# Kernel optimization log

Hardware: AMD Instinct MI355X
Metric: run time of the kernel (lower is better)

## Reference

```python
import jax, jax.numpy as jnp
import numpy as np

H = 16          # num_heads (init kwarg)
EPS = 1e-6      # LayerNorm eps


def rope_freqs(L, d):
    # interleaved RoPE freqs, repeat(f, 'i j -> i (j r)', r=2)
    t = jnp.arange(L, dtype=jnp.float32)
    inv = 1.0 / (10000.0 ** (jnp.arange(0, d, 2, dtype=jnp.float32) / d))
    f = t[:, None] * inv[None, :]          # (L, d//2)
    return jnp.repeat(f, 2, axis=-1)       # (L, d)


def rotate_half(x):
    # pair adjacent elems: (x1, x2) -> (-x2, x1)
    shp = x.shape
    x = x.reshape(shp[:-1] + (shp[-1] // 2, 2))
    x1, x2 = x[..., 0], x[..., 1]
    return jnp.stack((-x2, x1), axis=-1).reshape(shp)


def apply_rope(x, f):
    # x: (B, H, L, d), f: (L, d)
    return x * jnp.cos(f) + rotate_half(x) * jnp.sin(f)


def layernorm(x, g, b):
    m = jnp.mean(x, axis=-1, keepdims=True)
    v = jnp.mean(jnp.square(x - m), axis=-1, keepdims=True)
    return (x - m) * jax.lax.rsqrt(v + EPS) * g + b


def setup_inputs() -> dict:
    key = jax.random.key(0)
    ks = jax.random.split(key, 12)
    B, L, D = 2, 2048, 1024
    Dff = 4 * D
    s = 0.02
    inp = {
        'x': jax.random.normal(ks[0], (B, L, D), jnp.float32),
        'ln1_g': jnp.ones((D,), jnp.float32),
        'ln1_b': jnp.zeros((D,), jnp.float32),
        'wq': jax.random.normal(ks[1], (D, D), jnp.float32) * s,
        'bq': jnp.zeros((D,), jnp.float32),
        'wk': jax.random.normal(ks[2], (D, D), jnp.float32) * s,
        'bk': jnp.zeros((D,), jnp.float32),
        'wv': jax.random.normal(ks[3], (D, D), jnp.float32) * s,
        'bv': jnp.zeros((D,), jnp.float32),
        'wo': jax.random.normal(ks[4], (D, D), jnp.float32) * s,
        'bo': jnp.zeros((D,), jnp.float32),
        'ln2_g': jnp.ones((D,), jnp.float32),
        'ln2_b': jnp.zeros((D,), jnp.float32),
        'w1': jax.random.normal(ks[5], (D, Dff), jnp.float32) * s,
        'b1': jnp.zeros((Dff,), jnp.float32),
        'w2': jax.random.normal(ks[6], (Dff, D), jnp.float32) * s,
        'b2': jnp.zeros((D,), jnp.float32),
        # gates are zero-init in the module; use small random so the block is exercised
        'gate_msa': jax.random.normal(ks[7], (1, 1, D), jnp.float32) * 0.1,
        'gate_mlp': jax.random.normal(ks[8], (1, 1, D), jnp.float32) * 0.1,
    }
    return inp


def reference(x, ln1_g, ln1_b, wq, bq, wk, bk, wv, bv, wo, bo,
              ln2_g, ln2_b, w1, b1, w2, b2, gate_msa, gate_mlp):
    B, L, D = x.shape
    hd = D // H
    # --- self-attention branch ---
    h = layernorm(x, ln1_g, ln1_b)
    q = (h @ wq + bq).reshape(B, L, H, hd).transpose(0, 2, 1, 3)  # (B,H,L,hd)
    k = (h @ wk + bk).reshape(B, L, H, hd).transpose(0, 2, 1, 3)
    v = (h @ wv + bv).reshape(B, L, H, hd).transpose(0, 2, 1, 3)
    f = rope_freqs(L, hd)
    q = apply_rope(q, f)
    k = apply_rope(k, f)
    scores = jnp.einsum('bhic,bhjc->bhij', q, k) / np.float32(np.sqrt(hd))
    attn = jax.nn.softmax(scores, axis=-1)  # dropout disabled (eval)
    o = jnp.einsum('bhij,bhjc->bhic', attn, v)
    o = o.transpose(0, 2, 1, 3).reshape(B, L, D)
    x = x + gate_msa * (o @ wo + bo)
    # --- gated MLP branch ---
    h2 = layernorm(x, ln2_g, ln2_b)
    mlp = jax.nn.gelu(h2 @ w1 + b1, approximate=False) @ w2 + b2
    return x + gate_mlp * mlp
```

## Files before the change

kernel.cpp:

```cpp
#include <hip/hip_runtime.h>

typedef unsigned short u16;
typedef __attribute__((ext_vector_type(4))) float f32x4;
typedef __attribute__((ext_vector_type(16))) float f32x16;
typedef __attribute__((ext_vector_type(8))) short bf16x8;

#define DEV static __device__ __forceinline__

DEV float bf2f(u16 u) { unsigned int i = ((unsigned int)u) << 16; return __builtin_bit_cast(float, i); }
DEV u16 f2bf(float f) {
  unsigned int x = __builtin_bit_cast(unsigned int, f);
  x += 0x7fffu + ((x >> 16) & 1u);
  return (u16)(x >> 16);
}

DEV unsigned cvtpk(float lo, float hi) {
  unsigned r;
  asm("v_cvt_pk_bf16_f32 %0, %1, %2" : "=v"(r) : "v"(lo), "v"(hi));
  return r;
}
DEV float exp2a(float x) {
  float r;
  asm("v_exp_f32 %0, %1" : "=v"(r) : "v"(x));
  return r;
}

template <int N>
DEV void wait_vmcnt() {
  if constexpr (N == 0) asm volatile("s_waitcnt vmcnt(0)" ::: "memory");
  else if constexpr (N == 3) asm volatile("s_waitcnt vmcnt(3)" ::: "memory");
  else if constexpr (N == 4) asm volatile("s_waitcnt vmcnt(4)" ::: "memory");
  else static_assert(N == 0, "unsupported vmcnt");
}

DEV void gload16(const u16* g, u16* l) {
  __builtin_amdgcn_global_load_lds(
      (const __attribute__((address_space(1))) unsigned int*)g,
      (__attribute__((address_space(3))) unsigned int*)l, 16, 0, 0);
}

__global__ __launch_bounds__(256) void ln_k(const float* __restrict__ x,
                                            const float* __restrict__ g,
                                            const float* __restrict__ b,
                                            u16* __restrict__ out) {
  const int row = blockIdx.x;
  const int t = threadIdx.x;
  const float4 v = *(const float4*)(x + (size_t)row * 1024 + t * 4);
  float s = v.x + v.y + v.z + v.w;
  float q = v.x * v.x + v.y * v.y + v.z * v.z + v.w * v.w;
#pragma unroll
  for (int m = 1; m < 64; m <<= 1) { s += __shfl_xor(s, m); q += __shfl_xor(q, m); }
  __shared__ float ss[4], qs[4];
  if ((t & 63) == 0) { ss[t >> 6] = s; qs[t >> 6] = q; }
  __syncthreads();
  s = ss[0] + ss[1] + ss[2] + ss[3];
  q = qs[0] + qs[1] + qs[2] + qs[3];
  const float mean = s * (1.0f / 1024.0f);
  const float var = q * (1.0f / 1024.0f) - mean * mean;
  const float rs = rsqrtf(var + 1e-6f);
  const float4 gv = *(const float4*)(g + t * 4);
  const float4 bv = *(const float4*)(b + t * 4);
  ushort4 o;
  o.x = f2bf((v.x - mean) * rs * gv.x + bv.x);
  o.y = f2bf((v.y - mean) * rs * gv.y + bv.y);
  o.z = f2bf((v.z - mean) * rs * gv.z + bv.z);
  o.w = f2bf((v.w - mean) * rs * gv.w + bv.w);
  *(ushort4*)(out + (size_t)row * 1024 + t * 4) = o;
}

__global__ __launch_bounds__(256) void tcvt_k(const float* __restrict__ src,
                                              u16* __restrict__ dst, int K, int N) {
  __shared__ u16 tl[32][33];
  const int k0 = blockIdx.x * 32, n0 = blockIdx.y * 32;
  const int c = threadIdx.x & 31, r0 = threadIdx.x >> 5;
#pragma unroll
  for (int p = 0; p < 4; p++) {
    const int r = p * 8 + r0;
    tl[r][c] = f2bf(src[(size_t)(k0 + r) * N + n0 + c]);
  }
  __syncthreads();
#pragma unroll
  for (int p = 0; p < 4; p++) {
    const int r = p * 8 + r0;
    dst[(size_t)(n0 + r) * K + k0 + c] = tl[c][r];
  }
}

template <int EPI, int TN>
__global__ __launch_bounds__(256) void gemm_bt(const u16* __restrict__ A,
                                               const u16* __restrict__ Bt,
                                               const float* __restrict__ bias,
                                               const float* __restrict__ resid,
                                               const float* __restrict__ gate,
                                               void* __restrict__ outv,
                                               int M, int N, int K) {
  constexpr int MI = (TN == 128) ? 4 : 2;
  constexpr int WRS = (TN == 128) ? 64 : 32;
  constexpr int L = 2 + TN / 64;
  __shared__ __align__(16) u16 lA[3][128 * 32];
  __shared__ __align__(16) u16 lB[3][TN * 32];
  const int tid = threadIdx.x;
  const int lane = tid & 63, wid = tid >> 6;
  const int l4 = lane >> 4, l15 = lane & 15;
  const int wr = (TN == 128) ? (wid >> 1) : wid;
  const int wc = (TN == 128) ? (wid & 1) : 0;
  const int mBase = blockIdx.x * 128;
  const int nBase = blockIdx.y * TN;

  f32x4 acc[MI][4];
#pragma unroll
  for (int i = 0; i < MI; i++)
#pragma unroll
    for (int j = 0; j < 4; j++)
#pragma unroll
      for (int e = 0; e < 4; e++) acc[i][j][e] = 0.f;

  const int sRow = tid >> 2;
  const int sCol = (((tid & 3) ^ ((sRow >> 1) & 3))) * 8;
  const int rsw = (l15 >> 1) & 3;

#define STAGE(bufi, k0)                                                               \
  {                                                                                   \
    _Pragma("unroll") for (int p = 0; p < 2; p++)                                     \
        gload16(A + (size_t)(mBase + p * 64 + sRow) * K + (k0) + sCol,                \
                &lA[bufi][p * 2048 + wid * 512]);                                     \
    _Pragma("unroll") for (int p = 0; p < TN / 64; p++)                               \
        gload16(Bt + (size_t)(nBase + p * 64 + sRow) * K + (k0) + sCol,               \
                &lB[bufi][p * 2048 + wid * 512]);                                     \
  }

  const int nt = K >> 5;
  STAGE(0, 0);
  STAGE(1, 32);
  wait_vmcnt<L>();
  __builtin_amdgcn_s_barrier();
  __builtin_amdgcn_sched_barrier(0);

  int bsel = 0;
  for (int it = 0; it < nt; ++it) {
    bf16x8 af[MI], bfr[4];
#pragma unroll
    for (int mi = 0; mi < MI; mi++)
      af[mi] = *(const bf16x8*)(&lA[bsel][(wr * WRS + mi * 16 + l15) * 32 + (l4 ^ rsw) * 8]);
#pragma unroll
    for (int ni = 0; ni < 4; ni++)
      bfr[ni] = *(const bf16x8*)(&lB[bsel][(wc * 64 + ni * 16 + l15) * 32 + (l4 ^ rsw) * 8]);
    if (it + 2 < nt) {
      int b2 = bsel + 2; if (b2 >= 3) b2 -= 3;
      STAGE(b2, (it + 2) * 32);
    }
#pragma unroll
    for (int mi = 0; mi < MI; mi++)
#pragma unroll
      for (int ni = 0; ni < 4; ni++)
        acc[mi][ni] = __builtin_amdgcn_mfma_f32_16x16x32_bf16(af[mi], bfr[ni], acc[mi][ni], 0, 0, 0);
    if (it + 1 < nt) {
      asm volatile("s_waitcnt lgkmcnt(0)" ::: "memory");
      __builtin_amdgcn_sched_barrier(0);
      if (it + 2 < nt) wait_vmcnt<L>();
      else wait_vmcnt<0>();
      __builtin_amdgcn_s_barrier();
      __builtin_amdgcn_sched_barrier(0);
    }
    bsel = (bsel == 2) ? 0 : bsel + 1;
  }
#undef STAGE

  u16* obf = (u16*)outv;
  float* of = (float*)outv;
#pragma unroll
  for (int mi = 0; mi < MI; mi++) {
#pragma unroll
    for (int ni = 0; ni < 4; ni++) {
      const int row0 = mBase + wr * WRS + mi * 16 + l4 * 4;
      const int col = nBase + wc * 64 + ni * 16 + l15;
      const float bb = bias[col];
#pragma unroll
      for (int r = 0; r < 4; r++) {
        const float v = acc[mi][ni][r] + bb;
        const size_t idx = (size_t)(row0 + r) * N + col;
        if (EPI == 0) {
          obf[idx] = f2bf(v);
        } else if (EPI == 1) {
          const float ge = 0.5f * v * (1.0f + erff(v * 0.70710678118654752f));
          obf[idx] = f2bf(ge);
        } else if (EPI == 2) {
          of[idx] = resid[idx] + gate[col] * v;
        } else {
          of[idx] = of[idx] + gate[col] * v;
        }
      }
    }
  }
}

__global__ __launch_bounds__(256) void rope_k(const u16* __restrict__ qkv,
                                              u16* __restrict__ qr, u16* __restrict__ kr) {
  const int sel = blockIdx.y;
  const int rid = blockIdx.x * 8 + (threadIdx.x >> 5);
  const int i = threadIdx.x & 31;
  const int b = rid >> 15;
  const int h = (rid >> 11) & 15;
  const int t = rid & 2047;
  const u16* src = qkv + (size_t)(b * 2048 + t) * 3072 + sel * 1024 + h * 64 + 2 * i;
  const ushort2 uv = *(const ushort2*)src;
  const float x0 = bf2f(uv.x), x1 = bf2f(uv.y);
  const float inv = __expf(-(float)i * 0.28782313662425572f);
  float sn, cs;
  sincosf((float)t * inv, &sn, &cs);
  const float sc = sel ? 1.0f : 0.18033688011112042f;
  ushort2 ov;
  ov.x = f2bf((x0 * cs - x1 * sn) * sc);
  ov.y = f2bf((x1 * cs + x0 * sn) * sc);
  *(ushort2*)((sel ? kr : qr) + (size_t)rid * 64 + 2 * i) = ov;
}

__global__ __launch_bounds__(256) void vtrans_k(const u16* __restrict__ qkv, u16* __restrict__ vt) {
  __shared__ u16 tl[64][65];
  const int bh = blockIdx.x >> 5;
  const int t0 = (blockIdx.x & 31) * 64;
  const int b = bh >> 4, h = bh & 15;
  const int tid = threadIdx.x;
#pragma unroll
  for (int p = 0; p < 16; p++) {
    const int e = p * 256 + tid;
    const int tr = e >> 6, d = e & 63;
    tl[tr][d] = qkv[(size_t)(b * 2048 + t0 + tr) * 3072 + 2048 + h * 64 + d];
  }
  __syncthreads();
#pragma unroll
  for (int p = 0; p < 16; p++) {
    const int e = p * 256 + tid;
    const int dr = e >> 6, tc = e & 63;
    vt[(size_t)(bh * 64 + dr) * 2048 + t0 + tc] = tl[tc][dr];
  }
}

__global__ __launch_bounds__(256) void attn_k(const u16* __restrict__ q,
                                              const u16* __restrict__ k,
                                              const u16* __restrict__ vt,
                                              u16* __restrict__ o) {
  const int bh = blockIdx.y;
  const int tid = threadIdx.x;
  const int wid = tid >> 6, lane = tid & 63;
  const int h = lane >> 5, rq = lane & 31;
  const int qrow0 = blockIdx.x * 128 + wid * 32;

  __shared__ __align__(16) u16 kls[2][4096];
  __shared__ __align__(16) u16 vls[2][4096];
  __shared__ __align__(16) float alds[4][32];

  const u16* qbase = q + ((size_t)bh * 2048 + qrow0 + rq) * 64 + 8 * h;
  bf16x8 qf[4];
#pragma unroll
  for (int db = 0; db < 4; db++) qf[db] = *(const bf16x8*)(qbase + db * 16);

  float m0 = -1e30f, ls0 = 0.f;
  f32x16 oacc0, oacc1;
#pragma unroll
  for (int e = 0; e < 16; e++) { oacc0[e] = 0.f; oacc1[e] = 0.f; }

  const char* kg = (const char*)(k + (size_t)bh * 2048 * 64);
  const char* vg = (const char*)(vt + (size_t)bh * 64 * 2048);
  const int sA = tid, sB = 256 + tid;
  const int rA = sA >> 3, cA = ((sA & 7) ^ (rA & 7)) << 4;
  const int rB = sB >> 3, cB = ((sB & 7) ^ (rB & 7)) << 4;
  u16* kd0 = &kls[0][(size_t)(wid * 64) * 8];
  u16* kd1 = &kls[0][(size_t)(256 + wid * 64) * 8];
  u16* vd0 = &vls[0][(size_t)(wid * 64) * 8];
  u16* vd1 = &vls[0][(size_t)(256 + wid * 64) * 8];

#define STAGE(bufi, kv0)                                                            \
  {                                                                                 \
    const int _o = (bufi)*4096;                                                     \
    gload16((const u16*)(kg + (size_t)((kv0) + rA) * 128 + cA), kd0 + _o);          \
    gload16((const u16*)(kg + (size_t)((kv0) + rB) * 128 + cB), kd1 + _o);          \
    gload16((const u16*)(vg + (size_t)rA * 4096 + (kv0)*2 + cA), vd0 + _o);         \
    gload16((const u16*)(vg + (size_t)rB * 4096 + (kv0)*2 + cB), vd1 + _o);         \
  }

  STAGE(0, 0);
  __syncthreads();

  float* AL = alds[wid];
  const int swz = (rq & 7) << 4;

#define PACK8(S, B, OUT)                                                            \
  {                                                                                 \
    unsigned wA = cvtpk(S[B + 0], S[B + 1]), wB_ = cvtpk(S[B + 2], S[B + 3]);       \
    unsigned wC = cvtpk(S[B + 4], S[B + 5]), wD = cvtpk(S[B + 6], S[B + 7]);        \
    unsigned xA = __shfl_xor(wA, 32), xB = __shfl_xor(wB_, 32);                     \
    unsigned xC = __shfl_xor(wC, 32), xD = __shfl_xor(wD, 32);                      \
    union { unsigned u[4]; bf16x8 v; } _m;                                          \
    _m.u[0] = h ? xC : wA; _m.u[1] = h ? xD : wB_;                                  \
    _m.u[2] = h ? wC : xA; _m.u[3] = h ? wD : xB;                                   \
    OUT = _m.v;                                                                     \
  }

  int buf = 0;
  for (int it = 0; it < 32; ++it) {
    if (it < 31) STAGE(buf ^ 1, (it + 1) * 64);
    const char* K = (const char*)kls[buf];
    const char* V = (const char*)vls[buf];

    f32x16 st0, st1;
#pragma unroll
    for (int e = 0; e < 16; e++) { st0[e] = 0.f; st1[e] = 0.f; }
#pragma unroll
    for (int db = 0; db < 4; db++) {
      const int cb = db * 32;
      const bf16x8 ka0 = *(const bf16x8*)(K + rq * 128 + ((cb + 16 * h) ^ swz));
      const bf16x8 ka1 = *(const bf16x8*)(K + (32 + rq) * 128 + ((cb + 16 * h) ^ swz));
      st0 = __builtin_amdgcn_mfma_f32_32x32x16_bf16(ka0, qf[db], st0, 0, 0, 0);
      st1 = __builtin_amdgcn_mfma_f32_32x32x16_bf16(ka1, qf[db], st1, 0, 0, 0);
    }

    float t0 = fmaxf(fmaxf(st0[0], st0[1]), fmaxf(st0[2], st0[3]));
    float t1 = fmaxf(fmaxf(st0[4], st0[5]), fmaxf(st0[6], st0[7]));
    float t2 = fmaxf(fmaxf(st0[8], st0[9]), fmaxf(st0[10], st0[11]));
    float t3 = fmaxf(fmaxf(st0[12], st0[13]), fmaxf(st0[14], st0[15]));
    float t4 = fmaxf(fmaxf(st1[0], st1[1]), fmaxf(st1[2], st1[3]));
    float t5 = fmaxf(fmaxf(st1[4], st1[5]), fmaxf(st1[6], st1[7]));
    float t6 = fmaxf(fmaxf(st1[8], st1[9]), fmaxf(st1[10], st1[11]));
    float t7 = fmaxf(fmaxf(st1[12], st1[13]), fmaxf(st1[14], st1[15]));
    float pm = fmaxf(fmaxf(fmaxf(t0, t1), fmaxf(t2, t3)), fmaxf(fmaxf(t4, t5), fmaxf(t6, t7)));
    pm = fmaxf(pm, __shfl_xor(pm, 32));
    const bool need = !__all(pm <= m0 + 11.54f);
    float al0 = 1.0f;
    if (need) {
      const float mn = fmaxf(m0, pm);
      al0 = exp2a(m0 - mn);
      m0 = mn;
    }
#pragma unroll
    for (int e = 0; e < 16; e++) {
      st0[e] = exp2a(st0[e] - m0);
      st1[e] = exp2a(st1[e] - m0);
    }
    float u0 = (st0[0] + st0[1]) + (st0[2] + st0[3]);
    float u1 = (st0[4] + st0[5]) + (st0[6] + st0[7]);
    float u2 = (st0[8] + st0[9]) + (st0[10] + st0[11]);
    float u3 = (st0[12] + st0[13]) + (st0[14] + st0[15]);
    float u4 = (st1[0] + st1[1]) + (st1[2] + st1[3]);
    float u5 = (st1[4] + st1[5]) + (st1[6] + st1[7]);
    float u6 = (st1[8] + st1[9]) + (st1[10] + st1[11]);
    float u7 = (st1[12] + st1[13]) + (st1[14] + st1[15]);
    float ps = ((u0 + u1) + (u2 + u3)) + ((u4 + u5) + (u6 + u7));
    ps += __shfl_xor(ps, 32);
    ls0 = ls0 * al0 + ps;

    if (need) {
      if (lane < 32) AL[rq] = al0;
      const f32x4 a0 = *(const f32x4*)((const char*)AL + 16 * h);
      const f32x4 a1 = *(const f32x4*)((const char*)AL + 32 + 16 * h);
      const f32x4 a2 = *(const f32x4*)((const char*)AL + 64 + 16 * h);
      const f32x4 a3 = *(const f32x4*)((const char*)AL + 96 + 16 * h);
#pragma unroll
      for (int r = 0; r < 4; r++) {
        oacc0[r] *= a0[r]; oacc0[4 + r] *= a1[r]; oacc0[8 + r] *= a2[r]; oacc0[12 + r] *= a3[r];
        oacc1[r] *= a0[r]; oacc1[4 + r] *= a1[r]; oacc1[8 + r] *= a2[r]; oacc1[12 + r] *= a3[r];
      }
    }

    bf16x8 pa[4];
    PACK8(st0, 0, pa[0]);
    PACK8(st0, 8, pa[1]);
    PACK8(st1, 0, pa[2]);
    PACK8(st1, 8, pa[3]);

#pragma unroll
    for (int kb = 0; kb < 4; kb++) {
      const int cb = kb * 32;
      const bf16x8 vb0 = *(const bf16x8*)(V + rq * 128 + ((cb + 16 * h) ^ swz));
      const bf16x8 vb1 = *(const bf16x8*)(V + (32 + rq) * 128 + ((cb + 16 * h) ^ swz));
      oacc0 = __builtin_amdgcn_mfma_f32_32x32x16_bf16(pa[kb], vb0, oacc0, 0, 0, 0);
      oacc1 = __builtin_amdgcn_mfma_f32_32x32x16_bf16(pa[kb], vb1, oacc1, 0, 0, 0);
    }
    __syncthreads();
    buf ^= 1;
  }
#undef STAGE
#undef PACK8

  if (lane < 32) AL[rq] = 1.0f / ls0;
  f32x4 ivg[4];
  ivg[0] = *(const f32x4*)((const char*)AL + 16 * h);
  ivg[1] = *(const f32x4*)((const char*)AL + 32 + 16 * h);
  ivg[2] = *(const f32x4*)((const char*)AL + 64 + 16 * h);
  ivg[3] = *(const f32x4*)((const char*)AL + 96 + 16 * h);
  const int b = bh >> 4, hh = bh & 15;
#pragma unroll
  for (int r = 0; r < 16; r++) {
    const int qa = qrow0 + (r & 3) + 8 * (r >> 2) + 4 * h;
    u16* orow = o + ((size_t)b * 2048 + qa) * 1024 + hh * 64;
    const float iv = ivg[r >> 2][r & 3];
    orow[rq] = f2bf(oacc0[r] * iv);
    orow[32 + rq] = f2bf(oacc1[r] * iv);
  }
}

extern "C" void kernel_launch(void* const* d_in, const int* in_sizes, int n_in,
                              void* d_out, int out_size, void* d_ws, size_t ws_size,
                              hipStream_t stream) {
  (void)in_sizes; (void)n_in; (void)out_size; (void)ws_size;
  const float* x     = (const float*)d_in[0];
  const float* ln1_g = (const float*)d_in[1];
  const float* ln1_b = (const float*)d_in[2];
  const float* wq    = (const float*)d_in[3];
  const float* bq    = (const float*)d_in[4];
  const float* wk    = (const float*)d_in[5];
  const float* bk    = (const float*)d_in[6];
  const float* wv    = (const float*)d_in[7];
  const float* bv    = (const float*)d_in[8];
  const float* wo    = (const float*)d_in[9];
  const float* bo    = (const float*)d_in[10];
  const float* ln2_g = (const float*)d_in[11];
  const float* ln2_b = (const float*)d_in[12];
  const float* w1    = (const float*)d_in[13];
  const float* b1    = (const float*)d_in[14];
  const float* w2    = (const float*)d_in[15];
  const float* b2    = (const float*)d_in[16];
  const float* gmsa  = (const float*)d_in[17];
  const float* gmlp  = (const float*)d_in[18];
  float* out = (float*)d_out;

  char* w = (char*)d_ws;
  auto alloc = [&](size_t bytes) {
    char* p = w;
    w += (bytes + 255) & ~(size_t)255;
    return p;
  };
  u16* h1     = (u16*)alloc(4096UL * 1024 * 2);
  u16* wqkv_t = (u16*)alloc(3072UL * 1024 * 2);
  u16* wo_t   = (u16*)alloc(1024UL * 1024 * 2);
  u16* w1_t   = (u16*)alloc(4096UL * 1024 * 2);
  u16* w2_t   = (u16*)alloc(1024UL * 4096 * 2);
  float* bqkv = (float*)alloc(3072UL * 4);
  u16* qkv    = (u16*)alloc(4096UL * 3072 * 2);
  u16* q_r    = (u16*)alloc(65536UL * 64 * 2);
  u16* k_r    = (u16*)alloc(65536UL * 64 * 2);
  u16* v_t    = (u16*)alloc(65536UL * 64 * 2);
  u16* o_at   = (u16*)alloc(4096UL * 1024 * 2);
  u16* h2     = (u16*)alloc(4096UL * 1024 * 2);
  u16* g1     = (u16*)alloc(4096UL * 4096 * 2);

  tcvt_k<<<dim3(32, 32), 256, 0, stream>>>(wq, wqkv_t, 1024, 1024);
  tcvt_k<<<dim3(32, 32), 256, 0, stream>>>(wk, wqkv_t + 1024 * 1024, 1024, 1024);
  tcvt_k<<<dim3(32, 32), 256, 0, stream>>>(wv, wqkv_t + 2048 * 1024, 1024, 1024);
  tcvt_k<<<dim3(32, 32), 256, 0, stream>>>(wo, wo_t, 1024, 1024);
  tcvt_k<<<dim3(32, 128), 256, 0, stream>>>(w1, w1_t, 1024, 4096);
  tcvt_k<<<dim3(128, 32), 256, 0, stream>>>(w2, w2_t, 4096, 1024);
  hipMemcpyAsync(bqkv,        bq, 1024 * sizeof(float), hipMemcpyDeviceToDevice, stream);
  hipMemcpyAsync(bqkv + 1024, bk, 1024 * sizeof(float), hipMemcpyDeviceToDevice, stream);
  hipMemcpyAsync(bqkv + 2048, bv, 1024 * sizeof(float), hipMemcpyDeviceToDevice, stream);

  ln_k<<<4096, 256, 0, stream>>>(x, ln1_g, ln1_b, h1);
  gemm_bt<0, 128><<<dim3(32, 24), 256, 0, stream>>>(h1, wqkv_t, bqkv, nullptr, nullptr, qkv, 4096, 3072, 1024);
  rope_k<<<dim3(8192, 2), 256, 0, stream>>>(qkv, q_r, k_r);
  vtrans_k<<<1024, 256, 0, stream>>>(qkv, v_t);
  attn_k<<<dim3(16, 32), 256, 0, stream>>>(q_r, k_r, v_t, o_at);
  gemm_bt<2, 64><<<dim3(32, 16), 256, 0, stream>>>(o_at, wo_t, bo, x, gmsa, out, 4096, 1024, 1024);

  ln_k<<<4096, 256, 0, stream>>>(out, ln2_g, ln2_b, h2);
  gemm_bt<1, 128><<<dim3(32, 32), 256, 0, stream>>>(h2, w1_t, b1, nullptr, nullptr, g1, 4096, 4096, 1024);
  gemm_bt<3, 64><<<dim3(32, 16), 256, 0, stream>>>(g1, w2_t, b2, nullptr, gmlp, out, 4096, 1024, 4096);
}
```

Measured before the change: 286.3 us.

## Split attention KV range across two warp groups and merge softmax partials

The attention block grows to 512 threads: two groups of four waves each process half of the key/value sequence for the same 128 query rows, with separate double-buffered LDS tiles. At the end, group 1 writes its partial output, max and sum to shared memory, and group 0 rescales and combines both partials before storing. The aim is more waves per CU and a shorter serial KV loop for the 512-block grid. In exchange it doubles LDS use per block and adds a combine step with an extra barrier.

```diff
diff --git a/kernel.cpp b/kernel.cpp
--- a/kernel.cpp
+++ b/kernel.cpp
@@ -236,19 +236,22 @@
   }
 }
 
-__global__ __launch_bounds__(256) void attn_k(const u16* __restrict__ q,
+__global__ __launch_bounds__(512) void attn_k(const u16* __restrict__ q,
                                               const u16* __restrict__ k,
                                               const u16* __restrict__ vt,
                                               u16* __restrict__ o) {
   const int bh = blockIdx.y;
   const int tid = threadIdx.x;
-  const int wid = tid >> 6, lane = tid & 63;
+  const int grp = tid >> 8;
+  const int wid = (tid >> 6) & 3;
+  const int lane = tid & 63;
   const int h = lane >> 5, rq = lane & 31;
   const int qrow0 = blockIdx.x * 128 + wid * 32;
 
-  __shared__ __align__(16) u16 kls[2][4096];
-  __shared__ __align__(16) u16 vls[2][4096];
-  __shared__ __align__(16) float alds[4][32];
+  __shared__ __align__(16) u16 kls[2][2][4096];
+  __shared__ __align__(16) u16 vls[2][2][4096];
+  __shared__ __align__(16) float alds[8][32];
+  __shared__ __align__(16) float mls[4][32], lls[4][32];
 
   const u16* qbase = q + ((size_t)bh * 2048 + qrow0 + rq) * 64 + 8 * h;
   bf16x8 qf[4];
@@ -262,13 +265,17 @@
 
   const char* kg = (const char*)(k + (size_t)bh * 2048 * 64);
   const char* vg = (const char*)(vt + (size_t)bh * 64 * 2048);
-  const int sA = tid, sB = 256 + tid;
+  const int t8 = tid & 255;
+  const int sA = t8, sB = 256 + t8;
   const int rA = sA >> 3, cA = ((sA & 7) ^ (rA & 7)) << 4;
   const int rB = sB >> 3, cB = ((sB & 7) ^ (rB & 7)) << 4;
-  u16* kd0 = &kls[0][(size_t)(wid * 64) * 8];
-  u16* kd1 = &kls[0][(size_t)(256 + wid * 64) * 8];
-  u16* vd0 = &vls[0][(size_t)(wid * 64) * 8];
-  u16* vd1 = &vls[0][(size_t)(256 + wid * 64) * 8];
+  u16* kgrp = &kls[grp][0][0];
+  u16* vgrp = &vls[grp][0][0];
+  u16* kd0 = kgrp + wid * 512;
+  u16* kd1 = kgrp + 2048 + wid * 512;
+  u16* vd0 = vgrp + wid * 512;
+  u16* vd1 = vgrp + 2048 + wid * 512;
+  const int kvbase = grp * 1024;
 
 #define STAGE(bufi, kv0)                                                            \
   {                                                                                 \
@@ -279,10 +286,10 @@
     gload16((const u16*)(vg + (size_t)rB * 4096 + (kv0)*2 + cB), vd1 + _o);         \
   }
 
-  STAGE(0, 0);
+  STAGE(0, kvbase);
   __syncthreads();
 
-  float* AL = alds[wid];
+  float* AL = alds[tid >> 6];
   const int swz = (rq & 7) << 4;
 
 #define PACK8(S, B, OUT)                                                            \
@@ -298,10 +305,10 @@
   }
 
   int buf = 0;
-  for (int it = 0; it < 32; ++it) {
-    if (it < 31) STAGE(buf ^ 1, (it + 1) * 64);
-    const char* K = (const char*)kls[buf];
-    const char* V = (const char*)vls[buf];
+  for (int it = 0; it < 16; ++it) {
+    if (it < 15) STAGE(buf ^ 1, kvbase + (it + 1) * 64);
+    const char* K = (const char*)(kgrp + buf * 4096);
+    const char* V = (const char*)(vgrp + buf * 4096);
 
     f32x16 st0, st1;
 #pragma unroll
@@ -382,20 +389,41 @@
 #undef STAGE
 #undef PACK8
 
-  if (lane < 32) AL[rq] = 1.0f / ls0;
-  f32x4 ivg[4];
-  ivg[0] = *(const f32x4*)((const char*)AL + 16 * h);
-  ivg[1] = *(const f32x4*)((const char*)AL + 32 + 16 * h);
-  ivg[2] = *(const f32x4*)((const char*)AL + 64 + 16 * h);
-  ivg[3] = *(const f32x4*)((const char*)AL + 96 + 16 * h);
-  const int b = bh >> 4, hh = bh & 15;
-#pragma unroll
-  for (int r = 0; r < 16; r++) {
-    const int qa = qrow0 + (r & 3) + 8 * (r >> 2) + 4 * h;
-    u16* orow = o + ((size_t)b * 2048 + qa) * 1024 + hh * 64;
-    const float iv = ivg[r >> 2][r & 3];
-    orow[rq] = f2bf(oacc0[r] * iv);
-    orow[32 + rq] = f2bf(oacc1[r] * iv);
+  float* comb = (float*)&kls[0][0][0];
+  if (grp == 1) {
+    if (lane < 32) { mls[wid][rq] = m0; lls[wid][rq] = ls0; }
+    float* cw = comb + wid * 2048;
+#pragma unroll
+    for (int r = 0; r < 16; r++) {
+      const int ql = (r & 3) + 8 * (r >> 2) + 4 * h;
+      cw[ql * 64 + rq] = oacc0[r];
+      cw[ql * 64 + 32 + rq] = oacc1[r];
+    }
+  }
+  __syncthreads();
+  if (grp == 0) {
+    const float mb = mls[wid][rq], lb = lls[wid][rq];
+    const float M = fmaxf(m0, mb);
+    const float sa = exp2a(m0 - M), sb = exp2a(mb - M);
+    const float linv = 1.0f / (ls0 * sa + lb * sb);
+    if (lane < 32) { AL[rq] = sa * linv; mls[wid][rq] = sb * linv; }
+    asm volatile("s_waitcnt lgkmcnt(0)" ::: "memory");
+    f32x4 fa[4], fb[4];
+#pragma unroll
+    for (int g = 0; g < 4; g++) {
+      fa[g] = *(const f32x4*)((const char*)AL + g * 32 + 16 * h);
+      fb[g] = *(const f32x4*)((const char*)&mls[wid][0] + g * 32 + 16 * h);
+    }
+    const float* cw = comb + wid * 2048;
+    const int b = bh >> 4, hh = bh & 15;
+#pragma unroll
+    for (int r = 0; r < 16; r++) {
+      const int ql = (r & 3) + 8 * (r >> 2) + 4 * h;
+      const float A = fa[r >> 2][r & 3], B = fb[r >> 2][r & 3];
+      u16* orow = o + ((size_t)b * 2048 + qrow0 + ql) * 1024 + hh * 64;
+      orow[rq] = f2bf(oacc0[r] * A + cw[ql * 64 + rq] * B);
+      orow[32 + rq] = f2bf(oacc1[r] * A + cw[ql * 64 + 32 + rq] * B);
+    }
   }
 }
 
@@ -458,7 +486,7 @@
   gemm_bt<0, 128><<<dim3(32, 24), 256, 0, stream>>>(h1, wqkv_t, bqkv, nullptr, nullptr, qkv, 4096, 3072, 1024);
   rope_k<<<dim3(8192, 2), 256, 0, stream>>>(qkv, q_r, k_r);
   vtrans_k<<<1024, 256, 0, stream>>>(qkv, v_t);
-  attn_k<<<dim3(16, 32), 256, 0, stream>>>(q_r, k_r, v_t, o_at);
+  attn_k<<<dim3(16, 32), 512, 0, stream>>>(q_r, k_r, v_t, o_at);
   gemm_bt<2, 64><<<dim3(32, 16), 256, 0, stream>>>(o_at, wo_t, bo, x, gmsa, out, 4096, 1024, 1024);
 
   ln_k<<<4096, 256, 0, stream>>>(out, ln2_g, ln2_b, h2);
```

Measured after the change: 284.1 us. No clear change (-0.8%).

## Load K tiles straight into registers and double-buffer them across attention iterations

Applied to the files above, without the earlier changes.

The attention kernel no longer stages K through LDS. Each wave reads its K fragments directly from global memory into registers, one tile ahead, while V keeps its LDS double buffer. The loop is unrolled by two with ping-pong register buffers, explicit vmcnt/lgkmcnt waits and raw s_barrier. The MFMA sections are also wrapped in s_setprio. This is meant to cut LDS traffic and barrier cost, but every wave now fetches the same K tile separately, which raises global/L2 load traffic and register pressure.

```diff
diff --git a/kernel.cpp b/kernel.cpp
--- a/kernel.cpp
+++ b/kernel.cpp
@@ -30,6 +30,7 @@
   if constexpr (N == 0) asm volatile("s_waitcnt vmcnt(0)" ::: "memory");
   else if constexpr (N == 3) asm volatile("s_waitcnt vmcnt(3)" ::: "memory");
   else if constexpr (N == 4) asm volatile("s_waitcnt vmcnt(4)" ::: "memory");
+  else if constexpr (N == 8) asm volatile("s_waitcnt vmcnt(8)" ::: "memory");
   else static_assert(N == 0, "unsupported vmcnt");
 }
 
@@ -236,6 +237,121 @@
   }
 }
 
+#define PACK8(S, B, OUT, H)                                                         \
+  {                                                                                 \
+    unsigned wA = cvtpk(S[B + 0], S[B + 1]), wB_ = cvtpk(S[B + 2], S[B + 3]);       \
+    unsigned wC = cvtpk(S[B + 4], S[B + 5]), wD = cvtpk(S[B + 6], S[B + 7]);        \
+    unsigned xA = __shfl_xor(wA, 32), xB = __shfl_xor(wB_, 32);                     \
+    unsigned xC = __shfl_xor(wC, 32), xD = __shfl_xor(wD, 32);                      \
+    union { unsigned u[4]; bf16x8 v; } _m;                                          \
+    _m.u[0] = (H) ? xC : wA; _m.u[1] = (H) ? xD : wB_;                              \
+    _m.u[2] = (H) ? wC : xA; _m.u[3] = (H) ? wD : xB;                               \
+    OUT = _m.v;                                                                     \
+  }
+
+DEV void attn_iter(bool notlast, int kvnext,
+                   const u16* kgrow, const char* vg,
+                   int rA, int cA, int rB, int cB, u16* vdst0, u16* vdst1,
+                   const char* V, int swz, int h, int rq,
+                   const bf16x8 (&qf)[4], const bf16x8 (&kcur)[2][4], bf16x8 (&knxt)[2][4],
+                   float& m0, float& ls0, f32x16& oacc0, f32x16& oacc1, float* AL) {
+  if (notlast) {
+    gload16((const u16*)(vg + (size_t)rA * 4096 + (size_t)kvnext * 2 + cA), vdst0);
+    gload16((const u16*)(vg + (size_t)rB * 4096 + (size_t)kvnext * 2 + cB), vdst1);
+    __builtin_amdgcn_sched_barrier(0);
+    const u16* kb = kgrow + (size_t)kvnext * 64;
+#pragma unroll
+    for (int db = 0; db < 4; db++) {
+      knxt[0][db] = *(const bf16x8*)(kb + db * 16);
+      knxt[1][db] = *(const bf16x8*)(kb + 32 * 64 + db * 16);
+    }
+  }
+
+  f32x16 st0, st1;
+#pragma unroll
+  for (int e = 0; e < 16; e++) { st0[e] = 0.f; st1[e] = 0.f; }
+  __builtin_amdgcn_s_setprio(1);
+#pragma unroll
+  for (int db = 0; db < 4; db++) {
+    st0 = __builtin_amdgcn_mfma_f32_32x32x16_bf16(kcur[0][db], qf[db], st0, 0, 0, 0);
+    st1 = __builtin_amdgcn_mfma_f32_32x32x16_bf16(kcur[1][db], qf[db], st1, 0, 0, 0);
+  }
+  __builtin_amdgcn_s_setprio(0);
+
+  float t0 = fmaxf(fmaxf(st0[0], st0[1]), fmaxf(st0[2], st0[3]));
+  float t1 = fmaxf(fmaxf(st0[4], st0[5]), fmaxf(st0[6], st0[7]));
+  float t2 = fmaxf(fmaxf(st0[8], st0[9]), fmaxf(st0[10], st0[11]));
+  float t3 = fmaxf(fmaxf(st0[12], st0[13]), fmaxf(st0[14], st0[15]));
+  float t4 = fmaxf(fmaxf(st1[0], st1[1]), fmaxf(st1[2], st1[3]));
+  float t5 = fmaxf(fmaxf(st1[4], st1[5]), fmaxf(st1[6], st1[7]));
+  float t6 = fmaxf(fmaxf(st1[8], st1[9]), fmaxf(st1[10], st1[11]));
+  float t7 = fmaxf(fmaxf(st1[12], st1[13]), fmaxf(st1[14], st1[15]));
+  float pm = fmaxf(fmaxf(fmaxf(t0, t1), fmaxf(t2, t3)), fmaxf(fmaxf(t4, t5), fmaxf(t6, t7)));
+  pm = fmaxf(pm, __shfl_xor(pm, 32));
+  const bool need = !__all(pm <= m0 + 11.54f);
+  float al0 = 1.0f;
+  if (need) {
+    const float mn = fmaxf(m0, pm);
+    al0 = exp2a(m0 - mn);
+    m0 = mn;
+  }
+#pragma unroll
+  for (int e = 0; e < 16; e++) {
+    st0[e] = exp2a(st0[e] - m0);
+    st1[e] = exp2a(st1[e] - m0);
+  }
+  float u0 = (st0[0] + st0[1]) + (st0[2] + st0[3]);
+  float u1 = (st0[4] + st0[5]) + (st0[6] + st0[7]);
+  float u2 = (st0[8] + st0[9]) + (st0[10] + st0[11]);
+  float u3 = (st0[12] + st0[13]) + (st0[14] + st0[15]);
+  float u4 = (st1[0] + st1[1]) + (st1[2] + st1[3]);
+  float u5 = (st1[4] + st1[5]) + (st1[6] + st1[7]);
+  float u6 = (st1[8] + st1[9]) + (st1[10] + st1[11]);
+  float u7 = (st1[12] + st1[13]) + (st1[14] + st1[15]);
+  float ps = ((u0 + u1) + (u2 + u3)) + ((u4 + u5) + (u6 + u7));
+  ps += __shfl_xor(ps, 32);
+  ls0 = ls0 * al0 + ps;
+
+  if (need) {
+    const int lane = rq + 32 * h;
+    if (lane < 32) AL[rq] = al0;
+    const f32x4 a0 = *(const f32x4*)((const char*)AL + 16 * h);
+    const f32x4 a1 = *(const f32x4*)((const char*)AL + 32 + 16 * h);
+    const f32x4 a2 = *(const f32x4*)((const char*)AL + 64 + 16 * h);
+    const f32x4 a3 = *(const f32x4*)((const char*)AL + 96 + 16 * h);
+#pragma unroll
+    for (int r = 0; r < 4; r++) {
+      oacc0[r] *= a0[r]; oacc0[4 + r] *= a1[r]; oacc0[8 + r] *= a2[r]; oacc0[12 + r] *= a3[r];
+      oacc1[r] *= a0[r]; oacc1[4 + r] *= a1[r]; oacc1[8 + r] *= a2[r]; oacc1[12 + r] *= a3[r];
+    }
+  }
+
+  bf16x8 pa[4];
+  PACK8(st0, 0, pa[0], h);
+  PACK8(st0, 8, pa[1], h);
+  PACK8(st1, 0, pa[2], h);
+  PACK8(st1, 8, pa[3], h);
+
+  __builtin_amdgcn_s_setprio(1);
+#pragma unroll
+  for (int kb = 0; kb < 4; kb++) {
+    const int cb = kb * 32;
+    const bf16x8 vb0 = *(const bf16x8*)(V + rq * 128 + ((cb + 16 * h) ^ swz));
+    const bf16x8 vb1 = *(const bf16x8*)(V + (32 + rq) * 128 + ((cb + 16 * h) ^ swz));
+    oacc0 = __builtin_amdgcn_mfma_f32_32x32x16_bf16(pa[kb], vb0, oacc0, 0, 0, 0);
+    oacc1 = __builtin_amdgcn_mfma_f32_32x32x16_bf16(pa[kb], vb1, oacc1, 0, 0, 0);
+  }
+  __builtin_amdgcn_s_setprio(0);
+
+  if (notlast) {
+    asm volatile("s_waitcnt lgkmcnt(0)" ::: "memory");
+    __builtin_amdgcn_sched_barrier(0);
+    wait_vmcnt<8>();
+    __builtin_amdgcn_s_barrier();
+    __builtin_amdgcn_sched_barrier(0);
+  }
+}
+
 __global__ __launch_bounds__(256) void attn_k(const u16* __restrict__ q,
                                               const u16* __restrict__ k,
                                               const u16* __restrict__ vt,
@@ -246,7 +362,6 @@
   const int h = lane >> 5, rq = lane & 31;
   const int qrow0 = blockIdx.x * 128 + wid * 32;
 
-  __shared__ __align__(16) u16 kls[2][4096];
   __shared__ __align__(16) u16 vls[2][4096];
   __shared__ __align__(16) float alds[4][32];
 
@@ -260,127 +375,39 @@
 #pragma unroll
   for (int e = 0; e < 16; e++) { oacc0[e] = 0.f; oacc1[e] = 0.f; }
 
-  const char* kg = (const char*)(k + (size_t)bh * 2048 * 64);
+  const u16* kgrow = k + (size_t)bh * 2048 * 64 + (size_t)rq * 64 + 8 * h;
   const char* vg = (const char*)(vt + (size_t)bh * 64 * 2048);
   const int sA = tid, sB = 256 + tid;
   const int rA = sA >> 3, cA = ((sA & 7) ^ (rA & 7)) << 4;
   const int rB = sB >> 3, cB = ((sB & 7) ^ (rB & 7)) << 4;
-  u16* kd0 = &kls[0][(size_t)(wid * 64) * 8];
-  u16* kd1 = &kls[0][(size_t)(256 + wid * 64) * 8];
-  u16* vd0 = &vls[0][(size_t)(wid * 64) * 8];
-  u16* vd1 = &vls[0][(size_t)(256 + wid * 64) * 8];
-
-#define STAGE(bufi, kv0)                                                            \
-  {                                                                                 \
-    const int _o = (bufi)*4096;                                                     \
-    gload16((const u16*)(kg + (size_t)((kv0) + rA) * 128 + cA), kd0 + _o);          \
-    gload16((const u16*)(kg + (size_t)((kv0) + rB) * 128 + cB), kd1 + _o);          \
-    gload16((const u16*)(vg + (size_t)rA * 4096 + (kv0)*2 + cA), vd0 + _o);         \
-    gload16((const u16*)(vg + (size_t)rB * 4096 + (kv0)*2 + cB), vd1 + _o);         \
-  }
-
-  STAGE(0, 0);
-  __syncthreads();
-
+  u16* vd0 = &vls[0][wid * 512];
+  u16* vd1 = &vls[0][2048 + wid * 512];
   float* AL = alds[wid];
   const int swz = (rq & 7) << 4;
-
-#define PACK8(S, B, OUT)                                                            \
-  {                                                                                 \
-    unsigned wA = cvtpk(S[B + 0], S[B + 1]), wB_ = cvtpk(S[B + 2], S[B + 3]);       \
-    unsigned wC = cvtpk(S[B + 4], S[B + 5]), wD = cvtpk(S[B + 6], S[B + 7]);        \
-    unsigned xA = __shfl_xor(wA, 32), xB = __shfl_xor(wB_, 32);                     \
-    unsigned xC = __shfl_xor(wC, 32), xD = __shfl_xor(wD, 32);                      \
-    union { unsigned u[4]; bf16x8 v; } _m;                                          \
-    _m.u[0] = h ? xC : wA; _m.u[1] = h ? xD : wB_;                                  \
-    _m.u[2] = h ? wC : xA; _m.u[3] = h ? wD : xB;                                   \
-    OUT = _m.v;                                                                     \
-  }
-
-  int buf = 0;
-  for (int it = 0; it < 32; ++it) {
-    if (it < 31) STAGE(buf ^ 1, (it + 1) * 64);
-    const char* K = (const char*)kls[buf];
-    const char* V = (const char*)vls[buf];
-
-    f32x16 st0, st1;
-#pragma unroll
-    for (int e = 0; e < 16; e++) { st0[e] = 0.f; st1[e] = 0.f; }
-#pragma unroll
-    for (int db = 0; db < 4; db++) {
-      const int cb = db * 32;
-      const bf16x8 ka0 = *(const bf16x8*)(K + rq * 128 + ((cb + 16 * h) ^ swz));
-      const bf16x8 ka1 = *(const bf16x8*)(K + (32 + rq) * 128 + ((cb + 16 * h) ^ swz));
-      st0 = __builtin_amdgcn_mfma_f32_32x32x16_bf16(ka0, qf[db], st0, 0, 0, 0);
-      st1 = __builtin_amdgcn_mfma_f32_32x32x16_bf16(ka1, qf[db], st1, 0, 0, 0);
-    }
-
-    float t0 = fmaxf(fmaxf(st0[0], st0[1]), fmaxf(st0[2], st0[3]));
-    float t1 = fmaxf(fmaxf(st0[4], st0[5]), fmaxf(st0[6], st0[7]));
-    float t2 = fmaxf(fmaxf(st0[8], st0[9]), fmaxf(st0[10], st0[11]));
-    float t3 = fmaxf(fmaxf(st0[12], st0[13]), fmaxf(st0[14], st0[15]));
-    float t4 = fmaxf(fmaxf(st1[0], st1[1]), fmaxf(st1[2], st1[3]));
-    float t5 = fmaxf(fmaxf(st1[4], st1[5]), fmaxf(st1[6], st1[7]));
-    float t6 = fmaxf(fmaxf(st1[8], st1[9]), fmaxf(st1[10], st1[11]));
-    float t7 = fmaxf(fmaxf(st1[12], st1[13]), fmaxf(st1[14], st1[15]));
-    float pm = fmaxf(fmaxf(fmaxf(t0, t1), fmaxf(t2, t3)), fmaxf(fmaxf(t4, t5), fmaxf(t6, t7)));
-    pm = fmaxf(pm, __shfl_xor(pm, 32));
-    const bool need = !__all(pm <= m0 + 11.54f);
-    float al0 = 1.0f;
-    if (need) {
-      const float mn = fmaxf(m0, pm);
-      al0 = exp2a(m0 - mn);
-      m0 = mn;
-    }
-#pragma unroll
-    for (int e = 0; e < 16; e++) {
-      st0[e] = exp2a(st0[e] - m0);
-      st1[e] = exp2a(st1[e] - m0);
-    }
-    float u0 = (st0[0] + st0[1]) + (st0[2] + st0[3]);
-    float u1 = (st0[4] + st0[5]) + (st0[6] + st0[7]);
-    float u2 = (st0[8] + st0[9]) + (st0[10] + st0[11]);
-    float u3 = (st0[12] + st0[13]) + (st0[14] + st0[15]);
-    float u4 = (st1[0] + st1[1]) + (st1[2] + st1[3]);
-    float u5 = (st1[4] + st1[5]) + (st1[6] + st1[7]);
-    float u6 = (st1[8] + st1[9]) + (st1[10] + st1[11]);
-    float u7 = (st1[12] + st1[13]) + (st1[14] + st1[15]);
-    float ps = ((u0 + u1) + (u2 + u3)) + ((u4 + u5) + (u6 + u7));
-    ps += __shfl_xor(ps, 32);
-    ls0 = ls0 * al0 + ps;
-
-    if (need) {
-      if (lane < 32) AL[rq] = al0;
-      const f32x4 a0 = *(const f32x4*)((const char*)AL + 16 * h);
-      const f32x4 a1 = *(const f32x4*)((const char*)AL + 32 + 16 * h);
-      const f32x4 a2 = *(const f32x4*)((const char*)AL + 64 + 16 * h);
-      const f32x4 a3 = *(const f32x4*)((const char*)AL + 96 + 16 * h);
-#pragma unroll
-      for (int r = 0; r < 4; r++) {
-        oacc0[r] *= a0[r]; oacc0[4 + r] *= a1[r]; oacc0[8 + r] *= a2[r]; oacc0[12 + r] *= a3[r];
-        oacc1[r] *= a0[r]; oacc1[4 + r] *= a1[r]; oacc1[8 + r] *= a2[r]; oacc1[12 + r] *= a3[r];
-      }
-    }
-
-    bf16x8 pa[4];
-    PACK8(st0, 0, pa[0]);
-    PACK8(st0, 8, pa[1]);
-    PACK8(st1, 0, pa[2]);
-    PACK8(st1, 8, pa[3]);
-
-#pragma unroll
-    for (int kb = 0; kb < 4; kb++) {
-      const int cb = kb * 32;
-      const bf16x8 vb0 = *(const bf16x8*)(V + rq * 128 + ((cb + 16 * h) ^ swz));
-      const bf16x8 vb1 = *(const bf16x8*)(V + (32 + rq) * 128 + ((cb + 16 * h) ^ swz));
-      oacc0 = __builtin_amdgcn_mfma_f32_32x32x16_bf16(pa[kb], vb0, oacc0, 0, 0, 0);
-      oacc1 = __builtin_amdgcn_mfma_f32_32x32x16_bf16(pa[kb], vb1, oacc1, 0, 0, 0);
-    }
-    __syncthreads();
-    buf ^= 1;
-  }
-#undef STAGE
-#undef PACK8
+  const char* V0 = (const char*)&vls[0][0];
+  const char* V1 = (const char*)&vls[1][0];
+
+  bf16x8 kA[2][4], kB[2][4];
+  gload16((const u16*)(vg + (size_t)rA * 4096 + cA), vd0);
+  gload16((const u16*)(vg + (size_t)rB * 4096 + cB), vd1);
+  __builtin_amdgcn_sched_barrier(0);
+#pragma unroll
+  for (int db = 0; db < 4; db++) {
+    kA[0][db] = *(const bf16x8*)(kgrow + db * 16);
+    kA[1][db] = *(const bf16x8*)(kgrow + 32 * 64 + db * 16);
+  }
+  wait_vmcnt<8>();
+  __builtin_amdgcn_s_barrier();
+  __builtin_amdgcn_sched_barrier(0);
+
+  for (int it = 0; it < 32; it += 2) {
+    attn_iter(true, (it + 1) * 64, kgrow, vg, rA, cA, rB, cB,
+              vd0 + 4096, vd1 + 4096, V0, swz, h, rq, qf, kA, kB,
+              m0, ls0, oacc0, oacc1, AL);
+    attn_iter(it + 2 < 32, (it + 2) * 64, kgrow, vg, rA, cA, rB, cB,
+              vd0, vd1, V1, swz, h, rq, qf, kB, kA,
+              m0, ls0, oacc0, oacc1, AL);
+  }
 
   if (lane < 32) AL[rq] = 1.0f / ls0;
   f32x4 ivg[4];
```

Result: slower. 298.0 us (+4.1%).
